# Kernel optimization log

Hardware: AMD Instinct MI355X
Metric: run time of the kernel (lower is better)

Reference implementation:

```python
import jax, jax.numpy as jnp
import numpy as np

DIM = 256
QK = 256
HEADS = 8
NWIN = 16
TOPK = 4
MLP_RATIO = 4
SCALE = QK ** -0.5


def setup_inputs() -> dict:
    key = jax.random.key(0)
    ks = jax.random.split(key, 8)
    p = lambda k, shp: jax.random.normal(k, shp, jnp.float32) * 0.02
    hid = MLP_RATIO * DIM
    return {
        "x": jax.random.normal(ks[0], (8, DIM, 64, 64), jnp.float32),
        # to_q / to_kv : 1x1 Conv2d_BN (eval-mode BN with running stats 0/1 -> scale+shift)
        "wq": p(ks[1], (QK, DIM)), "gq": jnp.ones((QK,), jnp.float32), "bq": jnp.zeros((QK,), jnp.float32),
        "wkv": p(ks[2], (QK + DIM, DIM)), "gkv": jnp.ones((QK + DIM,), jnp.float32), "bkv": jnp.zeros((QK + DIM,), jnp.float32),
        # LEPE depthwise 5x5 conv
        "w_lepe": p(ks[3], (DIM, 1, 5, 5)), "b_lepe": jnp.zeros((DIM,), jnp.float32),
        # Mlp: fc1(1x1 Conv2d_BN) -> dwconv3x3 -> ReLU -> fc2(1x1 Conv2d_BN)
        "w_fc1": p(ks[4], (hid, DIM)), "g_fc1": jnp.ones((hid,), jnp.float32), "b_fc1": jnp.zeros((hid,), jnp.float32),
        "w_dw": p(ks[5], (hid, 1, 3, 3)), "b_dw": jnp.zeros((hid,), jnp.float32),
        "w_fc2": p(ks[6], (DIM, hid)), "g_fc2": jnp.ones((DIM,), jnp.float32), "b_fc2": jnp.zeros((DIM,), jnp.float32),
    }


def _dwconv(x, w, b, pad):
    # x: NCHW, w: (C,1,k,k) depthwise
    out = jax.lax.conv_general_dilated(
        x, w, (1, 1), [(pad, pad), (pad, pad)],
        feature_group_count=x.shape[1],
        dimension_numbers=("NCHW", "OIHW", "NCHW"))
    return out + b[None, :, None, None]


def _bra(x, wq, gq, bq, wkv, gkv, bkv, w_lepe, b_lepe):
    # Bi-Level Routing Attention. x: NCHW
    N, C, H, W = x.shape
    j = i = NWIN
    h, w_ = H // j, W // i          # per-window spatial (4,4)
    p2, w2 = j * i, h * w_          # 256 windows, 16 tokens/window
    xh = x.transpose(0, 2, 3, 1)    # NHWC
    # windowize: (N, p2, h, w, C)
    xw = xh.reshape(N, j, h, i, w_, C).transpose(0, 1, 3, 2, 4, 5).reshape(N, p2, h, w_, C)
    # 1x1 conv + BN(eval: stats 0/1) == matmul * gamma + beta
    q = (xw @ wq.T) * gq + bq                    # (N,p2,h,w,QK)
    kv = (xw @ wkv.T) * gkv + bkv                # (N,p2,h,w,QK+C)
    q_pix = q.reshape(N, p2, w2, QK)
    kv_pix = kv.reshape(N, p2, w2, QK + C)       # identity kv_down
    q_win = q.mean((2, 3))                       # (N,p2,QK)
    k_win = kv[..., :QK].mean((2, 3))            # (N,p2,QK)
    # LEPE on V in full-image layout
    v_img = kv[..., QK:].reshape(N, j, i, h, w_, C).transpose(0, 1, 3, 2, 4, 5).reshape(N, H, W, C)
    lepe = _dwconv(v_img.transpose(0, 3, 1, 2), w_lepe, b_lepe, 2).transpose(0, 2, 3, 1)  # NHWC
    # window-level topk routing (detached, non-differentiable)
    qd = jax.lax.stop_gradient(q_win)
    kd = jax.lax.stop_gradient(k_win)
    logit = (qd * SCALE) @ kd.transpose(0, 2, 1)            # (N,p2,p2)
    _, r_idx = jax.lax.top_k(logit, TOPK)                   # (N,p2,TOPK); r_weight unused (mul_weight='none')
    # gather selected KV windows: (N,p2,TOPK,w2,QK+C)
    kv_sel = jax.vmap(lambda kvp, idx: kvp[idx])(kv_pix, r_idx)
    ch_k, ch_v = QK // HEADS, C // HEADS
    k_sel = kv_sel[..., :QK].reshape(N, p2, TOPK * w2, HEADS, ch_k).transpose(0, 1, 3, 2, 4)
    v_sel = kv_sel[..., QK:].reshape(N, p2, TOPK * w2, HEADS, ch_v).transpose(0, 1, 3, 2, 4)
    qh = q_pix.reshape(N, p2, w2, HEADS, ch_k).transpose(0, 1, 3, 2, 4)
    attn = jax.nn.softmax(jnp.einsum("npmqc,npmkc->npmqk", qh * SCALE, k_sel), axis=-1)
    out = jnp.einsum("npmqk,npmkc->npmqc", attn, v_sel)     # (N,p2,HEADS,w2,ch_v)
    out = out.transpose(0, 1, 3, 2, 4).reshape(N, j, i, h, w_, C)
    out = out.transpose(0, 1, 3, 2, 4, 5).reshape(N, H, W, C)
    out = out + lepe                                         # wo = Identity
    return out.transpose(0, 3, 1, 2)                         # NCHW


def reference(x, wq, gq, bq, wkv, gkv, bkv, w_lepe, b_lepe,
              w_fc1, g_fc1, b_fc1, w_dw, b_dw, w_fc2, g_fc2, b_fc2):
    # top_Block: x = x + attn(x); x = x + mlp(x)   (drop_path inactive in eval)
    x = x + _bra(x, wq, gq, bq, wkv, gkv, bkv, w_lepe, b_lepe)
    h1 = jnp.einsum("nchw,dc->ndhw", x, w_fc1) * g_fc1[None, :, None, None] + b_fc1[None, :, None, None]
    h1 = jax.nn.relu(_dwconv(h1, w_dw, b_dw, 1))
    h2 = jnp.einsum("nchw,dc->ndhw", h1, w_fc2) * g_fc2[None, :, None, None] + b_fc2[None, :, None, None]
    return x + h2
```

## Files before the change

kernel.cpp:

```cpp
#include <hip/hip_runtime.h>
#include <hip/hip_bf16.h>

#define NBATCH 8
#define CDIM 256
#define HH 64
#define WW 64
#define HWSZ 4096
#define TT 32768
#define QKVD 768
#define TOPK 4
#define HID 1024
#define ATTN_SCALE 0.0625f

typedef __hip_bfloat16 bf16;
typedef __attribute__((ext_vector_type(8))) short s8v;
typedef __attribute__((ext_vector_type(4))) float f4v;

__device__ __forceinline__ float toF(bf16 v) { return __bfloat162float(v); }
__device__ __forceinline__ bf16  toB(float v) { return __float2bfloat16(v); }

__device__ __forceinline__ void gload_lds16(const bf16* g, bf16* l) {
    __builtin_amdgcn_global_load_lds(
        (const __attribute__((address_space(1))) void*)g,
        (__attribute__((address_space(3))) void*)l, 16, 0, 0);
}

__global__ void k_prep(const float* __restrict__ wq, const float* __restrict__ gq,
                       const float* __restrict__ wkv, const float* __restrict__ gkv,
                       const float* __restrict__ wfc1, const float* __restrict__ gfc1,
                       const float* __restrict__ wfc2, const float* __restrict__ gfc2,
                       const float* __restrict__ bq, const float* __restrict__ bkv,
                       const float* __restrict__ w_dw, const float* __restrict__ b_dw,
                       bf16* __restrict__ wbqkv, bf16* __restrict__ wbfc1,
                       bf16* __restrict__ wbfc2, float* __restrict__ bias768,
                       float* __restrict__ wdwT) {
    int i = blockIdx.x * 256 + threadIdx.x;
    if (i < 196608) {
        int r = i >> 8;
        float g = (r < 256) ? gq[r] : gkv[r - 256];
        float w = (r < 256) ? wq[i] : wkv[i - 65536];
        wbqkv[i] = toB(w * g);
        if (i < 768) bias768[i] = (i < 256) ? bq[i] : bkv[i - 256];
    } else if (i < 458752) {
        int j = i - 196608;
        wbfc1[j] = toB(wfc1[j] * gfc1[j >> 8]);
    } else if (i < 720896) {
        int j = i - 458752;
        wbfc2[j] = toB(wfc2[j] * gfc2[j >> 10]);
    } else if (i < 731136) {
        int j = i - 720896;
        int cg = j / 80, r = j - cg * 80;
        wdwT[j] = (r < 72) ? w_dw[(cg * 8 + r / 9) * 9 + (r % 9)]
                           : b_dw[cg * 8 + (r - 72)];
    }
}

__global__ void k_xt(const float* __restrict__ x, bf16* __restrict__ xt) {
    __shared__ float tile[32][33];
    int s0 = blockIdx.x * 32, c0 = blockIdx.y * 32, n = blockIdx.z;
    int tx = threadIdx.x, ty = threadIdx.y;
#pragma unroll
    for (int r = 0; r < 4; r++)
        tile[ty + r * 8][tx] = x[(size_t)n * CDIM * HWSZ + (size_t)(c0 + ty + r * 8) * HWSZ + s0 + tx];
    __syncthreads();
#pragma unroll
    for (int r = 0; r < 4; r++)
        xt[((size_t)n * HWSZ + s0 + ty + r * 8) * CDIM + c0 + tx] = toB(tile[tx][ty + r * 8]);
}

__global__ void k_xwin(const float* __restrict__ x, float* __restrict__ xwin) {
    int b = blockIdx.x;
    int n = b >> 8, c = b & 255;
    int p = threadIdx.x, wy = p >> 4, wx = p & 15;
    const float* pl = x + ((size_t)n * CDIM + c) * HWSZ;
    float s = 0.f;
#pragma unroll
    for (int dy = 0; dy < 4; dy++)
#pragma unroll
        for (int dx = 0; dx < 4; dx++)
            s += pl[(wy * 4 + dy) * WW + wx * 4 + dx];
    xwin[((size_t)(n << 8) + p) * 256 + c] = s * 0.0625f;
}

__global__ void k_qkwin(const float* __restrict__ xwin,
                        const float* __restrict__ wq, const float* __restrict__ wkv,
                        const float* __restrict__ gq, const float* __restrict__ bq,
                        const float* __restrict__ gkv, const float* __restrict__ bkv,
                        float* __restrict__ qkwin) {
    __shared__ float As[16][68];
    __shared__ float Bs[16][68];
    int m0 = blockIdx.x * 64, n0 = blockIdx.y * 64;
    int tid = threadIdx.x;
    int tx = tid & 15, ty = tid >> 4;
    float acc[4][4] = {};
    for (int k0 = 0; k0 < 256; k0 += 16) {
#pragma unroll
        for (int r = 0; r < 4; r++) {
            int lin = tid + r * 256;
            int row = lin >> 4, kk = lin & 15;
            As[kk][row] = xwin[(size_t)(m0 + row) * 256 + k0 + kk];
            int n = n0 + row;
            const float* wr = (n < 256) ? (wq + (size_t)n * 256) : (wkv + (size_t)(n - 256) * 256);
            Bs[kk][row] = wr[k0 + kk];
        }
        __syncthreads();
#pragma unroll
        for (int kk = 0; kk < 16; kk++) {
            float a[4], bb[4];
#pragma unroll
            for (int i = 0; i < 4; i++) a[i] = As[kk][tx * 4 + i];
#pragma unroll
            for (int j = 0; j < 4; j++) bb[j] = Bs[kk][ty * 4 + j];
#pragma unroll
            for (int i = 0; i < 4; i++)
#pragma unroll
                for (int j = 0; j < 4; j++) acc[i][j] += a[i] * bb[j];
        }
        __syncthreads();
    }
#pragma unroll
    for (int j = 0; j < 4; j++) {
        int n = n0 + ty * 4 + j;
        float gg = (n < 256) ? gq[n] : gkv[n - 256];
        float bb = (n < 256) ? bq[n] : bkv[n - 256];
#pragma unroll
        for (int i = 0; i < 4; i++)
            qkwin[(size_t)(m0 + tx * 4 + i) * 512 + n] = acc[i][j] * gg + bb;
    }
}

__global__ void k_logits(const float* __restrict__ qkwin, float* __restrict__ logits) {
    __shared__ float As[16][68];
    __shared__ float Bs[16][68];
    int m0 = blockIdx.x * 64, n0 = blockIdx.y * 64, img = blockIdx.z;
    const float* base = qkwin + (size_t)(img << 8) * 512;
    int tid = threadIdx.x;
    int tx = tid & 15, ty = tid >> 4;
    float acc[4][4] = {};
    for (int k0 = 0; k0 < 256; k0 += 16) {
#pragma unroll
        for (int r = 0; r < 4; r++) {
            int lin = tid + r * 256;
            int row = lin >> 4, kk = lin & 15;
            As[kk][row] = base[(size_t)(m0 + row) * 512 + k0 + kk];
            Bs[kk][row] = base[(size_t)(n0 + row) * 512 + 256 + k0 + kk];
        }
        __syncthreads();
#pragma unroll
        for (int kk = 0; kk < 16; kk++) {
            float a[4], bb[4];
#pragma unroll
            for (int i = 0; i < 4; i++) a[i] = As[kk][tx * 4 + i];
#pragma unroll
            for (int j = 0; j < 4; j++) bb[j] = Bs[kk][ty * 4 + j];
#pragma unroll
            for (int i = 0; i < 4; i++)
#pragma unroll
                for (int j = 0; j < 4; j++) acc[i][j] += a[i] * bb[j];
        }
        __syncthreads();
    }
    float* Lr = logits + (size_t)(img << 8) * 256;
#pragma unroll
    for (int j = 0; j < 4; j++)
#pragma unroll
        for (int i = 0; i < 4; i++)
            Lr[(size_t)(m0 + tx * 4 + i) * 256 + n0 + ty * 4 + j] = acc[i][j];
}

__global__ __launch_bounds__(256) void k_topk(const float* __restrict__ logits,
                                              int* __restrict__ topk) {
    int row = blockIdx.x * 4 + (threadIdx.x >> 6);
    int lane = threadIdx.x & 63;
    float4 v4 = *(const float4*)(logits + (size_t)row * 256 + lane * 4);
    float v[4] = {v4.x, v4.y, v4.z, v4.w};
#pragma unroll
    for (int sel = 0; sel < TOPK; sel++) {
        float mv = v[0]; int mi = lane * 4;
#pragma unroll
        for (int j = 1; j < 4; j++)
            if (v[j] > mv) { mv = v[j]; mi = lane * 4 + j; }
#pragma unroll
        for (int off = 1; off < 64; off <<= 1) {
            float ov = __shfl_xor(mv, off);
            int oi = __shfl_xor(mi, off);
            if (ov > mv || (ov == mv && oi < mi)) { mv = ov; mi = oi; }
        }
        if (lane == 0) topk[(size_t)row * TOPK + sel] = mi;
        if ((mi >> 2) == lane) v[mi & 3] = -INFINITY;
    }
}

template <int BM, int BN>
__global__ __launch_bounds__(256) void k_mfma(const bf16* __restrict__ A,
                                              const bf16* __restrict__ Wb,
                                              const float* __restrict__ bias,
                                              bf16* __restrict__ out,
                                              int M, int N, int K) {
    constexpr int WROWS = BM / 2, WCOLS = BN / 2;
    constexpr int WM = WROWS / 16, WN = WCOLS / 16;
    constexpr int CA = (BM * 4) / 256;
    constexpr int CB = (BN * 4) / 256;
    __shared__ bf16 As[BM * 32];
    __shared__ bf16 Bs[BN * 32];
    int gx = gridDim.x;
    int lin = blockIdx.x + blockIdx.y * gx;
    int tot = gx * gridDim.y;
    int cpx = tot >> 3;
    int swz = (lin & 7) * cpx + (lin >> 3);
    int m0 = (swz % gx) * BM, n0 = (swz / gx) * BN;
    int tid = threadIdx.x;
    int w = tid >> 6, lane = tid & 63;
    int wr = w >> 1, wc = w & 1;
    int lm = lane & 15, lq = lane >> 4;
    f4v acc[WM][WN];
#pragma unroll
    for (int i = 0; i < WM; i++)
#pragma unroll
        for (int j = 0; j < WN; j++) acc[i][j] = (f4v){0.f, 0.f, 0.f, 0.f};

    for (int k0 = 0; k0 < K; k0 += 32) {
#pragma unroll
        for (int q = 0; q < CA; q++) {
            int c = tid + q * 256, row = c >> 2, col = c & 3;
            gload_lds16(A + (size_t)(m0 + row) * K + k0 + col * 8,
                        As + (size_t)(w * 64 + q * 256) * 8);
        }
#pragma unroll
        for (int q = 0; q < CB; q++) {
            int c = tid + q * 256, row = c >> 2, col = c & 3;
            gload_lds16(Wb + (size_t)(n0 + row) * K + k0 + col * 8,
                        Bs + (size_t)(w * 64 + q * 256) * 8);
        }
        asm volatile("s_waitcnt vmcnt(0)" ::: "memory");
        __syncthreads();
        s8v af[WM], bfr[WN];
#pragma unroll
        for (int i = 0; i < WM; i++)
            af[i] = *(const s8v*)&As[(wr * WROWS + i * 16 + lm) * 32 + lq * 8];
#pragma unroll
        for (int j = 0; j < WN; j++)
            bfr[j] = *(const s8v*)&Bs[(wc * WCOLS + j * 16 + lm) * 32 + lq * 8];
#pragma unroll
        for (int i = 0; i < WM; i++)
#pragma unroll
            for (int j = 0; j < WN; j++)
                acc[i][j] = __builtin_amdgcn_mfma_f32_16x16x32_bf16(af[i], bfr[j], acc[i][j], 0, 0, 0);
        __syncthreads();
    }
#pragma unroll
    for (int j = 0; j < WN; j++) {
        int n = n0 + wc * WCOLS + j * 16 + lm;
        float bb = bias[n];
#pragma unroll
        for (int i = 0; i < WM; i++) {
            int mb = m0 + wr * WROWS + i * 16 + lq * 4;
#pragma unroll
            for (int r = 0; r < 4; r++)
                out[(size_t)(mb + r) * N + n] = toB(acc[i][j][r] + bb);
        }
    }
}

__global__ __launch_bounds__(256) void k_lepe_t(const bf16* __restrict__ qkv,
                                                const float* __restrict__ w_lepe,
                                                const float* __restrict__ b_lepe,
                                                bf16* __restrict__ lepe) {
    __shared__ float lw[25 * 64 * 4];
    int tid = threadIdx.x;
    int cg = tid & 63;
    int slot = tid >> 6;
    int b = blockIdx.x;
    int n = b & 7;
    int bx = b >> 3;
    int y = bx >> 1;
    int x0 = (bx & 1) * 32 + slot * 8;
#pragma unroll
    for (int j = 0; j < 25; j++) {
        int g = tid + j * 256;
        float val = w_lepe[g];
        int ch = g / 25, k = g - ch * 25;
        lw[(k * 64 + (ch >> 2)) * 4 + (ch & 3)] = val;
    }
    float4 b4 = *(const float4*)(b_lepe + cg * 4);
    const float* bias4 = (const float*)&b4;
    __syncthreads();
    const bf16* vb = qkv + (size_t)n * HWSZ * QKVD + 512;
    bf16* dst = lepe + (size_t)n * HWSZ * CDIM;
    float o[8][4];
#pragma unroll
    for (int xi = 0; xi < 8; xi++)
#pragma unroll
        for (int c = 0; c < 4; c++) o[xi][c] = bias4[c];
#pragma unroll
    for (int dy = -2; dy <= 2; dy++) {
        int yy = y + dy;
        if (yy < 0 || yy >= HH) continue;
        float rf[12][4];
#pragma unroll
        for (int ii = 0; ii < 12; ii++) {
            int xx = x0 - 2 + ii;
            if (xx >= 0 && xx < WW) {
                uint2 v = *(const uint2*)(vb + (size_t)(yy * WW + xx) * QKVD + cg * 4);
                const bf16* pv = (const bf16*)&v;
#pragma unroll
                for (int c = 0; c < 4; c++) rf[ii][c] = toF(pv[c]);
            } else {
#pragma unroll
                for (int c = 0; c < 4; c++) rf[ii][c] = 0.f;
            }
        }
#pragma unroll
        for (int dx = 0; dx < 5; dx++) {
            int k = (dy + 2) * 5 + dx;
            float4 w4v = *(const float4*)&lw[(k * 64 + cg) * 4];
            const float* w4 = (const float*)&w4v;
#pragma unroll
            for (int xi = 0; xi < 8; xi++)
#pragma unroll
                for (int c = 0; c < 4; c++) o[xi][c] += rf[xi + dx][c] * w4[c];
        }
    }
#pragma unroll
    for (int xi = 0; xi < 8; xi++) {
        uint2 pk;
        bf16* pb = (bf16*)&pk;
#pragma unroll
        for (int c = 0; c < 4; c++) pb[c] = toB(o[xi][c]);
        *(uint2*)(dst + (size_t)(y * WW + x0 + xi) * CDIM + cg * 4) = pk;
    }
}

__global__ __launch_bounds__(256) void k_attn(const bf16* __restrict__ qkv,
                                              const int* __restrict__ topk,
                                              const bf16* __restrict__ lepe,
                                              bf16* x1t) {
    __shared__ bf16 vst[256][72];
    __shared__ bf16 plds[4][16][72];
    __shared__ float lsm[4][16];
    __shared__ int toks[64];
    int b = blockIdx.x;
    int n = b & 7, p = b >> 3;
    int wy = p >> 4, wx = p & 15;
    int tid = threadIdx.x;
    if (tid < 64) {
        int rp = topk[((size_t)(n << 8) + p) * TOPK + (tid >> 4)] & 255;
        int st = tid & 15;
        toks[tid] = ((rp >> 4) * 4 + (st >> 2)) * WW + (rp & 15) * 4 + (st & 3);
    }
    __syncthreads();
    const bf16* qbase = qkv + (size_t)n * HWSZ * QKVD;
    {
        int kt = tid & 63, jj = tid >> 6;
#pragma unroll
        for (int pass = 0; pass < 8; pass++) {
            int d0 = pass * 32 + jj * 8;
            uint4 v = *(const uint4*)(qbase + (size_t)toks[kt] * QKVD + 512 + d0);
            const bf16* pv = (const bf16*)&v;
#pragma unroll
            for (int e = 0; e < 8; e++) vst[d0 + e][kt] = pv[e];
        }
    }
    __syncthreads();
    int w = tid >> 6, lane = tid & 63;
    int ln = lane & 15, lq = lane >> 4;
    int myS = (wy * 4 + (ln >> 2)) * WW + wx * 4 + (ln & 3);
    const f4v fz = {0.f, 0.f, 0.f, 0.f};
    for (int hh = 0; hh < 2; hh++) {
        int h = w * 2 + hh;
        s8v qf = *(const s8v*)(qbase + (size_t)myS * QKVD + h * 32 + lq * 8);
        f4v st4[4];
#pragma unroll
        for (int t = 0; t < 4; t++) {
            s8v kf = *(const s8v*)(qbase + (size_t)toks[t * 16 + ln] * QKVD + 256 + h * 32 + lq * 8);
            st4[t] = __builtin_amdgcn_mfma_f32_16x16x32_bf16(kf, qf, fz, 0, 0, 0);
        }
        float mx = -INFINITY;
#pragma unroll
        for (int t = 0; t < 4; t++)
#pragma unroll
            for (int r = 0; r < 4; r++) mx = fmaxf(mx, st4[t][r]);
        mx = fmaxf(mx, __shfl_xor(mx, 16));
        mx = fmaxf(mx, __shfl_xor(mx, 32));
        mx *= ATTN_SCALE;
        float sum = 0.f;
#pragma unroll
        for (int t = 0; t < 4; t++)
#pragma unroll
            for (int r = 0; r < 4; r++) {
                float pp = __expf(st4[t][r] * ATTN_SCALE - mx);
                sum += pp;
                plds[w][ln][t * 16 + lq * 4 + r] = toB(pp);
            }
        sum += __shfl_xor(sum, 16);
        sum += __shfl_xor(sum, 32);
        if (lq == 0) lsm[w][ln] = sum;
        __syncthreads();
        s8v ap0 = *(const s8v*)&plds[w][ln][lq * 8];
        s8v ap1 = *(const s8v*)&plds[w][ln][32 + lq * 8];
#pragma unroll
        for (int dt = 0; dt < 2; dt++) {
            int dim = h * 32 + dt * 16 + ln;
            s8v vv0 = *(const s8v*)&vst[dim][lq * 8];
            s8v vv1 = *(const s8v*)&vst[dim][32 + lq * 8];
            f4v o = __builtin_amdgcn_mfma_f32_16x16x32_bf16(ap0, vv0, fz, 0, 0, 0);
            o = __builtin_amdgcn_mfma_f32_16x16x32_bf16(ap1, vv1, o, 0, 0, 0);
#pragma unroll
            for (int r = 0; r < 4; r++) {
                int t = lq * 4 + r;
                float linv = 1.f / lsm[w][t];
                int s = (wy * 4 + (t >> 2)) * WW + wx * 4 + (t & 3);
                size_t idx = ((size_t)n * HWSZ + s) * CDIM + dim;
                x1t[idx] = toB(o[r] * linv + toF(x1t[idx]) + toF(lepe[idx]));
            }
        }
        __syncthreads();
    }
}

__global__ __launch_bounds__(256) void k_dw3_t(const bf16* __restrict__ h1,
                                               const float* __restrict__ wdwT,
                                               bf16* __restrict__ h1p) {
    int tid = threadIdx.x;
    int cg = tid & 127;
    int slot = tid >> 7;
    int lin = blockIdx.x;
    int img = lin & 7;
    int seg = lin >> 3;
    int y = seg >> 2;
    int x0 = ((seg & 3) << 4) + (slot << 3);
    const float* wp = wdwT + cg * 80;
    float w[72], bias[8];
#pragma unroll
    for (int i = 0; i < 72; i++) w[i] = wp[i];
#pragma unroll
    for (int c = 0; c < 8; c++) bias[c] = wp[72 + c];
    const uint4* src = (const uint4*)h1 + (size_t)img * HWSZ * 128;
    uint4* dst = (uint4*)h1p + (size_t)img * HWSZ * 128;
#pragma unroll
    for (int xi = 0; xi < 8; xi++) {
        int x = x0 + xi;
        float o[8];
#pragma unroll
        for (int c = 0; c < 8; c++) o[c] = bias[c];
#pragma unroll
        for (int dy = -1; dy <= 1; dy++) {
            int yy = y + dy;
            if (yy < 0 || yy >= HH) continue;
#pragma unroll
            for (int dx = -1; dx <= 1; dx++) {
                int xx = x + dx;
                if (xx < 0 || xx >= WW) continue;
                int k = (dy + 1) * 3 + (dx + 1);
                uint4 v = src[(size_t)(yy * WW + xx) * 128 + cg];
                const bf16* pv = (const bf16*)&v;
#pragma unroll
                for (int c = 0; c < 8; c++) o[c] += toF(pv[c]) * w[c * 9 + k];
            }
        }
        uint4 pk;
        bf16* pb = (bf16*)&pk;
#pragma unroll
        for (int c = 0; c < 8; c++) pb[c] = toB(fmaxf(o[c], 0.f));
        dst[(size_t)(y * WW + x) * 128 + cg] = pk;
    }
}

__global__ void k_final(const bf16* __restrict__ x1, const bf16* __restrict__ h2,
                        float* __restrict__ out) {
    __shared__ float tile[32][33];
    int s0 = blockIdx.x * 32, c0 = blockIdx.y * 32, n = blockIdx.z;
    int tx = threadIdx.x, ty = threadIdx.y;
#pragma unroll
    for (int r = 0; r < 4; r++) {
        int s = s0 + ty + r * 8;
        size_t idx = ((size_t)n * HWSZ + s) * CDIM + c0 + tx;
        tile[tx][ty + r * 8] = toF(x1[idx]) + toF(h2[idx]);
    }
    __syncthreads();
#pragma unroll
    for (int r = 0; r < 4; r++) {
        int c = c0 + ty + r * 8;
        out[(size_t)n * CDIM * HWSZ + (size_t)c * HWSZ + s0 + tx] = tile[ty + r * 8][tx];
    }
}

extern "C" void kernel_launch(void* const* d_in, const int* in_sizes, int n_in,
                              void* d_out, int out_size, void* d_ws, size_t ws_size,
                              hipStream_t stream) {
    (void)in_sizes; (void)n_in; (void)out_size; (void)ws_size;
    const float* x      = (const float*)d_in[0];
    const float* wq     = (const float*)d_in[1];
    const float* gq     = (const float*)d_in[2];
    const float* bq     = (const float*)d_in[3];
    const float* wkv    = (const float*)d_in[4];
    const float* gkv    = (const float*)d_in[5];
    const float* bkv    = (const float*)d_in[6];
    const float* w_lepe = (const float*)d_in[7];
    const float* b_lepe = (const float*)d_in[8];
    const float* w_fc1  = (const float*)d_in[9];
    const float* g_fc1  = (const float*)d_in[10];
    const float* b_fc1  = (const float*)d_in[11];
    const float* w_dw   = (const float*)d_in[12];
    const float* b_dw   = (const float*)d_in[13];
    const float* w_fc2  = (const float*)d_in[14];
    const float* g_fc2  = (const float*)d_in[15];
    const float* b_fc2  = (const float*)d_in[16];

    char* ws = (char*)d_ws;
    bf16*  qkv    = (bf16*)(ws);
    bf16*  lepe   = (bf16*)(ws + 50331648);
    bf16*  xt     = (bf16*)(ws + 67108864);
    bf16*  x1     = (bf16*)(ws + 67108864);
    bf16*  h1     = (bf16*)(ws + 83886080);
    bf16*  h1p    = (bf16*)(ws + 150994944);
    bf16*  h2     = (bf16*)(ws + 218103808);
    float* xwin   = (float*)(ws + 234881024);
    float* qkwin  = (float*)(ws + 236978176);
    float* logits = (float*)(ws + 241172480);
    int*   tk     = (int*)(ws + 243269632);
    bf16*  wbqkv  = (bf16*)(ws + 243302400);
    bf16*  wbfc1  = (bf16*)(ws + 243695616);
    bf16*  wbfc2  = (bf16*)(ws + 244219904);
    float* bias768= (float*)(ws + 244744192);
    float* wdwT   = (float*)(ws + 244747264);

    k_prep<<<2856, 256, 0, stream>>>(wq, gq, wkv, gkv, w_fc1, g_fc1, w_fc2, g_fc2,
                                     bq, bkv, w_dw, b_dw,
                                     wbqkv, wbfc1, wbfc2, bias768, wdwT);
    k_xt<<<dim3(128, 8, 8), dim3(32, 8), 0, stream>>>(x, xt);
    k_xwin<<<2048, 256, 0, stream>>>(x, xwin);
    k_qkwin<<<dim3(32, 8), 256, 0, stream>>>(xwin, wq, wkv, gq, bq, gkv, bkv, qkwin);
    k_logits<<<dim3(4, 4, 8), 256, 0, stream>>>(qkwin, logits);
    k_topk<<<512, 256, 0, stream>>>(logits, tk);
    k_mfma<128, 128><<<dim3(256, 6), 256, 0, stream>>>(
        xt, wbqkv, bias768, qkv, TT, QKVD, CDIM);
    k_lepe_t<<<1024, 256, 0, stream>>>(qkv, w_lepe, b_lepe, lepe);
    k_attn<<<2048, 256, 0, stream>>>(qkv, tk, lepe, x1);
    k_mfma<128, 128><<<dim3(256, 8), 256, 0, stream>>>(
        x1, wbfc1, b_fc1, h1, TT, HID, CDIM);
    k_dw3_t<<<2048, 256, 0, stream>>>(h1, wdwT, h1p);
    k_mfma<64, 128><<<dim3(512, 2), 256, 0, stream>>>(
        h1p, wbfc2, b_fc2, h2, TT, CDIM, HID);
    k_final<<<dim3(128, 8, 8), dim3(32, 8), 0, stream>>>(x1, h2, (float*)d_out);
}
```

Baseline: 405.6 us.

## Stage depthwise 3x3 weights in LDS and reuse row loads across taps

```diff
diff --git a/kernel.cpp b/kernel.cpp
--- a/kernel.cpp
+++ b/kernel.cpp
@@ -50,7 +50,7 @@
     } else if (i < 731136) {
         int j = i - 720896;
         int cg = j / 80, r = j - cg * 80;
-        wdwT[j] = (r < 72) ? w_dw[(cg * 8 + r / 9) * 9 + (r % 9)]
+        wdwT[j] = (r < 72) ? w_dw[(cg * 8 + (r & 7)) * 9 + (r >> 3)]
                            : b_dw[cg * 8 + (r - 72)];
     }
 }
@@ -421,7 +421,15 @@
 __global__ __launch_bounds__(256) void k_dw3_t(const bf16* __restrict__ h1,
                                                const float* __restrict__ wdwT,
                                                bf16* __restrict__ h1p) {
+    __shared__ float lw[128 * 81];
     int tid = threadIdx.x;
+#pragma unroll
+    for (int j = 0; j < 40; j++) {
+        int g = tid + j * 256;
+        int cgg = g / 80, r = g - cgg * 80;
+        lw[cgg * 81 + r] = wdwT[g];
+    }
+    __syncthreads();
     int cg = tid & 127;
     int slot = tid >> 7;
     int lin = blockIdx.x;
@@ -429,40 +437,61 @@
     int seg = lin >> 3;
     int y = seg >> 2;
     int x0 = ((seg & 3) << 4) + (slot << 3);
-    const float* wp = wdwT + cg * 80;
-    float w[72], bias[8];
-#pragma unroll
-    for (int i = 0; i < 72; i++) w[i] = wp[i];
-#pragma unroll
-    for (int c = 0; c < 8; c++) bias[c] = wp[72 + c];
+    const float* wl = lw + cg * 81;
+    float o[8][8];
+    {
+        float4 b0 = *(const float4*)&wl[72];
+        float4 b1 = *(const float4*)&wl[76];
+        const float* p0 = (const float*)&b0;
+        const float* p1 = (const float*)&b1;
+#pragma unroll
+        for (int xi = 0; xi < 8; xi++)
+#pragma unroll
+            for (int c = 0; c < 4; c++) { o[xi][c] = p0[c]; o[xi][c + 4] = p1[c]; }
+    }
     const uint4* src = (const uint4*)h1 + (size_t)img * HWSZ * 128;
     uint4* dst = (uint4*)h1p + (size_t)img * HWSZ * 128;
 #pragma unroll
-    for (int xi = 0; xi < 8; xi++) {
-        int x = x0 + xi;
-        float o[8];
-#pragma unroll
-        for (int c = 0; c < 8; c++) o[c] = bias[c];
-#pragma unroll
-        for (int dy = -1; dy <= 1; dy++) {
-            int yy = y + dy;
-            if (yy < 0 || yy >= HH) continue;
-#pragma unroll
-            for (int dx = -1; dx <= 1; dx++) {
-                int xx = x + dx;
-                if (xx < 0 || xx >= WW) continue;
-                int k = (dy + 1) * 3 + (dx + 1);
+    for (int dy = -1; dy <= 1; dy++) {
+        int yy = y + dy;
+        if (yy < 0 || yy >= HH) continue;
+        float rf[10][8];
+#pragma unroll
+        for (int ii = 0; ii < 10; ii++) {
+            int xx = x0 - 1 + ii;
+            if (xx >= 0 && xx < WW) {
                 uint4 v = src[(size_t)(yy * WW + xx) * 128 + cg];
                 const bf16* pv = (const bf16*)&v;
 #pragma unroll
-                for (int c = 0; c < 8; c++) o[c] += toF(pv[c]) * w[c * 9 + k];
+                for (int c = 0; c < 8; c++) rf[ii][c] = toF(pv[c]);
+            } else {
+#pragma unroll
+                for (int c = 0; c < 8; c++) rf[ii][c] = 0.f;
             }
         }
+#pragma unroll
+        for (int dx = 0; dx < 3; dx++) {
+            int k = (dy + 1) * 3 + dx;
+            float4 w0 = *(const float4*)&wl[k * 8];
+            float4 w1 = *(const float4*)&wl[k * 8 + 4];
+            const float* pw0 = (const float*)&w0;
+            const float* pw1 = (const float*)&w1;
+#pragma unroll
+            for (int xi = 0; xi < 8; xi++)
+#pragma unroll
+                for (int c = 0; c < 4; c++) {
+                    o[xi][c]     += rf[xi + dx][c]     * pw0[c];
+                    o[xi][c + 4] += rf[xi + dx][c + 4] * pw1[c];
+                }
+        }
+    }
+#pragma unroll
+    for (int xi = 0; xi < 8; xi++) {
         uint4 pk;
         bf16* pb = (bf16*)&pk;
 #pragma unroll
-        for (int c = 0; c < 8; c++) pb[c] = toB(fmaxf(o[c], 0.f));
-        dst[(size_t)(y * WW + x) * 128 + cg] = pk;
+        for (int c = 0; c < 8; c++) pb[c] = toB(fmaxf(o[xi][c], 0.f));
+        dst[(size_t)(y * WW + x0 + xi) * 128 + cg] = pk;
     }
 }
 
```

Result: faster. 397.2 us (-2.1%).
